# Kernel optimization log

Hardware: AMD Instinct MI355X
Metric: run time of the kernel (lower is better)

The kernel has to match this reference:

```python
import jax, jax.numpy as jnp
import numpy as np

B, T, D_MODEL, D_HEAD = 4, 4096, 512, 64  # batch, token_depth, token_len, d_head
D_K = 64
NEG = -1.0e9  # mask fill value used by the torch module


def setup_inputs() -> dict:
    key = jax.random.key(0)
    kx, kq, kk, kv = jax.random.split(key, 4)
    x = jax.random.normal(kx, (B, T, D_MODEL), dtype=jnp.float32)
    # nn.Linear(token_len, d_head, bias=False) -> weight shape [d_head, token_len]
    Wq = jax.random.normal(kq, (D_HEAD, D_MODEL), dtype=jnp.float32) * 0.02
    Wk = jax.random.normal(kk, (D_HEAD, D_MODEL), dtype=jnp.float32) * 0.02
    Wv = jax.random.normal(kv, (D_HEAD, D_MODEL), dtype=jnp.float32) * 0.02
    return {"x": x, "Wq": Wq, "Wk": Wk, "Wv": Wv}


def reference(x, Wq, Wk, Wv):
    # q/k/v projections: y = x @ W.T  (Linear with bias=False)
    q = jnp.einsum("btd,hd->bth", x, Wq)  # [B,T,D_HEAD]
    k = jnp.einsum("btd,hd->bth", x, Wk)
    v = jnp.einsum("btd,hd->bth", x, Wv)

    scores = jnp.einsum("bth,bsh->bts", q, k)  # [B,T,T]

    # additive causal mask: upper triangle (diagonal=1) filled with -1e9
    t_idx = jnp.arange(T)
    mask = jnp.where(t_idx[None, :] > t_idx[:, None], NEG, 0.0).astype(scores.dtype)
    scores = scores + mask[None, :, :]

    sqrt_dk = jnp.sqrt(jnp.asarray(D_K, dtype=scores.dtype))
    # NOTE: original code applies softmax over dim=1 (the query axis), not -1.
    attn = jax.nn.softmax(scores / sqrt_dk, axis=1)
    out = jnp.einsum("bts,bsh->bth", attn, v)  # [B,T,D_HEAD]
    return out
```

## Files before the change

kernel.cpp:

```cpp
#include <hip/hip_runtime.h>

#define B_ 4
#define T_ 4096
#define DM 512
#define DH 64
#define CS 512
#define CTS 512
#define NTASK 144

typedef short short8 __attribute__((ext_vector_type(8)));
typedef short bf16x4 __attribute__((ext_vector_type(4)));
typedef float f32x4 __attribute__((ext_vector_type(4)));
typedef float float8 __attribute__((ext_vector_type(8)));

__device__ inline short f2bf(float f) {
    unsigned u = __float_as_uint(f);
    u += 0x7fffu + ((u >> 16) & 1u);
    return (short)(u >> 16);
}
__device__ inline float bf2f(short s) {
    return __uint_as_float(((unsigned)(unsigned short)s) << 16);
}
__device__ inline short8 cvt8(const float* p) {
    float8 v = *(const float8*)p;
    short8 r;
#pragma unroll
    for (int j = 0; j < 8; j++) r[j] = f2bf(v[j]);
    return r;
}
__device__ inline unsigned cvt_pk_bf16(float a, float b) {
    unsigned r;
    asm("v_cvt_pk_bf16_f32 %0, %1, %2" : "=v"(r) : "v"(a), "v"(b));
    return r;
}
__device__ inline bf16x4 pmask4(f32x4 d, int sbase, int t) {
    float p[4];
#pragma unroll
    for (int r = 0; r < 4; r++) {
        float e = __expf(d[r] * 0.125f);
        p[r] = (sbase + r <= t) ? e : 0.f;
    }
    union { unsigned u[2]; bf16x4 v; } z;
    z.u[0] = cvt_pk_bf16(p[0], p[1]);
    z.u[1] = cvt_pk_bf16(p[2], p[3]);
    return z.v;
}

__global__ __launch_bounds__(256, 4) void k_proj(
    const float* __restrict__ x, const float* __restrict__ Wq,
    const float* __restrict__ Wk, const float* __restrict__ Wv,
    short* __restrict__ qb, short* __restrict__ kb, short* __restrict__ vb,
    float* __restrict__ lsum)
{
    __shared__ short Xs[16 * 72];
    __shared__ short Ws[192 * 72];
    int tid = threadIdx.x;
    int lane = tid & 63, w = tid >> 6;
    int l16 = lane & 15, quad = lane >> 4;
    int b = blockIdx.x >> 8;
    int tile = blockIdx.x & 255;
    int t0 = tile * 16;
    long xbase = ((long)(b * T_ + t0)) * DM;
    int hb = w * 3;

    if (tid < 16) lsum[blockIdx.x * 16 + tid] = 0.f;

    f32x4 acc[3];
#pragma unroll
    for (int i = 0; i < 3; i++) acc[i] = (f32x4)(0.f);

    for (int kc = 0; kc < DM; kc += 64) {
        if (tid < 128) {
            int row = tid >> 3, col = (tid & 7) * 8;
            *(short8*)(Xs + row * 72 + col) = cvt8(x + xbase + (long)row * DM + kc + col);
        }
#pragma unroll
        for (int p = 0; p < 6; p++) {
            int idx = p * 256 + tid;
            int row = idx >> 3, col = (idx & 7) * 8;
            const float* Wsrc = (p < 2) ? Wq : (p < 4) ? Wk : Wv;
            *(short8*)(Ws + row * 72 + col) = cvt8(Wsrc + (long)(row & 63) * DM + kc + col);
        }
        __syncthreads();
#pragma unroll
        for (int ks = 0; ks < 2; ks++) {
            short8 af = *(const short8*)(Xs + l16 * 72 + ks * 32 + quad * 8);
#pragma unroll
            for (int j = 0; j < 3; j++) {
                short8 bf = *(const short8*)(Ws + ((hb + j) * 16 + l16) * 72 + ks * 32 + quad * 8);
                acc[j] = __builtin_amdgcn_mfma_f32_16x16x32_bf16(af, bf, acc[j], 0, 0, 0);
            }
        }
        __syncthreads();
    }
#pragma unroll
    for (int j = 0; j < 3; j++) {
        int hh = hb + j, m = hh >> 2, h4 = hh & 3;
        short* outp = (m == 0) ? qb : (m == 1) ? kb : vb;
#pragma unroll
        for (int r4 = 0; r4 < 4; r4++) {
            int t = t0 + quad * 4 + r4;
            outp[((long)(b * T_ + t)) * DH + h4 * 16 + l16] = f2bf(acc[j][r4]);
        }
    }
}

__global__ __launch_bounds__(256, 4) void k_stats(
    const short* __restrict__ qb, const short* __restrict__ kb,
    float* __restrict__ lsum, float* __restrict__ out)
{
    __shared__ short Qb[128 * 72];
    int tid = threadIdx.x;
    int lane = tid & 63, w = tid >> 6;
    int l16 = lane & 15, quad = lane >> 4;

    {
        long idx = (long)blockIdx.x * 256 + tid;
        if (idx < 262144) *(f32x4*)(out + idx * 4) = (f32x4)(0.f);
        idx += (long)B_ * NTASK * 256;
        if (idx < 262144) *(f32x4*)(out + idx * 4) = (f32x4)(0.f);
    }

    int b = blockIdx.x / NTASK;
    int m = blockIdx.x - b * NTASK;
    int st = 0, chunk = 0;
    for (st = 0; st < 32; st++) {
        int cnt = 8 - (st >> 2);
        if (m < cnt) { chunk = (st >> 2) + m; break; }
        m -= cnt;
    }
    int c0 = chunk * CTS, cend = c0 + CTS;
    int s0blk = st * 128;
    int s0w = s0blk + w * 32;
    long bq = (long)b * T_ * DH;

    const short8* kp0 = (const short8*)(kb + bq + (long)(s0w + l16) * DH + quad * 8);
    short8 a00 = kp0[0], a01 = kp0[4];
    const short8* kp1 = (const short8*)(kb + bq + (long)(s0w + 16 + l16) * DH + quad * 8);
    short8 a10 = kp1[0], a11 = kp1[4];

    int t_lo = (c0 > s0blk) ? c0 : s0blk;
    int nsteps = (cend - t_lo) >> 7;
    float acc0[4] = {0.f, 0.f, 0.f, 0.f};
    float acc1[4] = {0.f, 0.f, 0.f, 0.f};

    for (int stp = 0; stp < nsteps; stp++) {
        int t0 = t_lo + stp * 128;
#pragma unroll
        for (int p = 0; p < 4; p++) {
            int idx = p * 256 + tid;
            int row = idx >> 3, col = idx & 7;
            *(short8*)(Qb + row * 72 + col * 8) =
                *(const short8*)(qb + bq + (long)(t0 + row) * DH + col * 8);
        }
        __syncthreads();
        for (int sub = 0; sub < 8; sub++) {
            int tt = t0 + sub * 16;
            if (tt + 15 >= s0w) {
                short8 b0 = *(const short8*)(Qb + (sub * 16 + l16) * 72 + quad * 8);
                short8 b1 = *(const short8*)(Qb + (sub * 16 + l16) * 72 + 32 + quad * 8);
                int t = tt + l16;
                f32x4 d0 = (f32x4)(0.f);
                d0 = __builtin_amdgcn_mfma_f32_16x16x32_bf16(a00, b0, d0, 0, 0, 0);
                d0 = __builtin_amdgcn_mfma_f32_16x16x32_bf16(a01, b1, d0, 0, 0, 0);
#pragma unroll
                for (int r = 0; r < 4; r++) {
                    int s = s0w + quad * 4 + r;
                    float p = __expf(d0[r] * 0.125f);
                    acc0[r] += (t >= s) ? p : 0.f;
                }
                if (tt + 15 >= s0w + 16) {
                    f32x4 d1 = (f32x4)(0.f);
                    d1 = __builtin_amdgcn_mfma_f32_16x16x32_bf16(a10, b0, d1, 0, 0, 0);
                    d1 = __builtin_amdgcn_mfma_f32_16x16x32_bf16(a11, b1, d1, 0, 0, 0);
#pragma unroll
                    for (int r = 0; r < 4; r++) {
                        int s = s0w + 16 + quad * 4 + r;
                        float p = __expf(d1[r] * 0.125f);
                        acc1[r] += (t >= s) ? p : 0.f;
                    }
                }
            }
        }
        __syncthreads();
    }
#pragma unroll
    for (int r = 0; r < 4; r++) {
        float v = acc0[r];
        v += __shfl_xor(v, 1, 16); v += __shfl_xor(v, 2, 16);
        v += __shfl_xor(v, 4, 16); v += __shfl_xor(v, 8, 16);
        if (l16 == 0) atomicAdd(&lsum[b * T_ + s0w + quad * 4 + r], v);
        float v1 = acc1[r];
        v1 += __shfl_xor(v1, 1, 16); v1 += __shfl_xor(v1, 2, 16);
        v1 += __shfl_xor(v1, 4, 16); v1 += __shfl_xor(v1, 8, 16);
        if (l16 == 0) atomicAdd(&lsum[b * T_ + s0w + 16 + quad * 4 + r], v1);
    }
}

__global__ __launch_bounds__(256) void k_vt(
    const short* __restrict__ vb, const float* __restrict__ lsum, short* __restrict__ vTc)
{
    int tid = threadIdx.x;
    int b = blockIdx.x >> 6;
    int s0 = (blockIdx.x & 63) * 64;
    int h = tid & 63, g = tid >> 6;
    long vbase = ((long)(b * T_) + s0 + g * 16) * DH + h;
    long lbase = (long)b * T_ + s0 + g * 16;
    short8 lo, hi;
#pragma unroll
    for (int k2 = 0; k2 < 8; k2++) {
        float rl = 1.0f / lsum[lbase + k2];
        lo[k2] = f2bf(bf2f(vb[vbase + (long)k2 * DH]) * rl);
        float rh = 1.0f / lsum[lbase + 8 + k2];
        hi[k2] = f2bf(bf2f(vb[vbase + (long)(8 + k2) * DH]) * rh);
    }
    long ob = ((long)(b * 256 + (s0 >> 4) + g) * 64 + h) * 16;
    *(short8*)(vTc + ob) = lo;
    *(short8*)(vTc + ob + 8) = hi;
}

__global__ __launch_bounds__(256, 4) void k_out(
    const short* __restrict__ qb, const short* __restrict__ kb,
    const short* __restrict__ vTc, float* __restrict__ out)
{
    __shared__ short Kb[128 * 72];
    int tid = threadIdx.x;
    int lane = tid & 63, w = tid >> 6;
    int l16 = lane & 15, quad = lane >> 4;
    int b = blockIdx.x / NTASK;
    int m = blockIdx.x - b * NTASK;
    int strip = 31, chunk = 0;
    for (strip = 31; strip >= 0; strip--) {
        int cnt = (strip >> 2) + 1;
        if (m < cnt) { chunk = m; break; }
        m -= cnt;
    }
    int c0 = chunk * CS;
    int blk_tmax = strip * 128 + 127;
    int s_hi = (c0 + CS < blk_tmax + 1) ? c0 + CS : blk_tmax + 1;
    int nsteps = (s_hi - c0 + 127) >> 7;
    int t0w = strip * 128 + w * 32;
    long bq = (long)b * T_ * DH;

    const short8* qp0 = (const short8*)(qb + bq + (long)(t0w + l16) * DH + quad * 8);
    short8 q00 = qp0[0], q01 = qp0[4];
    const short8* qp1 = (const short8*)(qb + bq + (long)(t0w + 16 + l16) * DH + quad * 8);
    short8 q10 = qp1[0], q11 = qp1[4];
    const short* vTb = vTc + (long)b * (T_ / 16) * DH * 16;

    f32x4 o0[4], o1[4];
#pragma unroll
    for (int i = 0; i < 4; i++) { o0[i] = (f32x4)(0.f); o1[i] = (f32x4)(0.f); }
    int t0 = t0w + l16, t1 = t0 + 16;

    for (int stp = 0; stp < nsteps; stp++) {
        int s0 = c0 + stp * 128;
#pragma unroll
        for (int p = 0; p < 4; p++) {
            int idx = p * 256 + tid;
            int row = idx >> 3, col = idx & 7;
            *(short8*)(Kb + row * 72 + col * 8) =
                *(const short8*)(kb + bq + (long)(s0 + row) * DH + col * 8);
        }
        __syncthreads();

        for (int sub = 0; sub < 8; sub++) {
            int sc = s0 + sub * 16;
            if (sc > t0w + 31) break;
            short8 a0 = *(const short8*)(Kb + (sub * 16 + l16) * 72 + quad * 8);
            short8 a1 = *(const short8*)(Kb + (sub * 16 + l16) * 72 + 32 + quad * 8);
            const short* vc = vTb + (long)(sc >> 4) * 1024 + quad * 4;
            bf16x4 bv[4];
#pragma unroll
            for (int h4 = 0; h4 < 4; h4++)
                bv[h4] = *(const bf16x4*)(vc + (h4 * 16 + l16) * 16);

            f32x4 d1 = (f32x4)(0.f);
            d1 = __builtin_amdgcn_mfma_f32_16x16x32_bf16(a0, q10, d1, 0, 0, 0);
            d1 = __builtin_amdgcn_mfma_f32_16x16x32_bf16(a1, q11, d1, 0, 0, 0);
            bf16x4 pa1 = pmask4(d1, sc + quad * 4, t1);

            bf16x4 pa0 = (bf16x4)(short)0;
            if (sc <= t0w + 15) {
                f32x4 d0 = (f32x4)(0.f);
                d0 = __builtin_amdgcn_mfma_f32_16x16x32_bf16(a0, q00, d0, 0, 0, 0);
                d0 = __builtin_amdgcn_mfma_f32_16x16x32_bf16(a1, q01, d0, 0, 0, 0);
                pa0 = pmask4(d0, sc + quad * 4, t0);
            }
#pragma unroll
            for (int h4 = 0; h4 < 4; h4++) {
                o1[h4] = __builtin_amdgcn_mfma_f32_16x16x16bf16_1k(pa1, bv[h4], o1[h4], 0, 0, 0);
                o0[h4] = __builtin_amdgcn_mfma_f32_16x16x16bf16_1k(pa0, bv[h4], o0[h4], 0, 0, 0);
            }
        }
        __syncthreads();
    }
#pragma unroll
    for (int h4 = 0; h4 < 4; h4++)
#pragma unroll
        for (int r = 0; r < 4; r++) {
            int t = t0w + quad * 4 + r;
            atomicAdd(&out[bq + (long)t * DH + h4 * 16 + l16], o0[h4][r]);
            atomicAdd(&out[bq + (long)(t + 16) * DH + h4 * 16 + l16], o1[h4][r]);
        }
}

extern "C" void kernel_launch(void* const* d_in, const int* in_sizes, int n_in,
                              void* d_out, int out_size, void* d_ws, size_t ws_size,
                              hipStream_t stream) {
    const float* x  = (const float*)d_in[0];
    const float* Wq = (const float*)d_in[1];
    const float* Wk = (const float*)d_in[2];
    const float* Wv = (const float*)d_in[3];
    float* out = (float*)d_out;

    char* ws = (char*)d_ws;
    short* qb   = (short*)(ws);
    short* kb   = (short*)(ws + (2l << 20));
    short* vb   = (short*)(ws + (4l << 20));
    short* vTc  = (short*)(ws + (6l << 20));
    float* lsum = (float*)(ws + (8l << 20));

    k_proj<<<dim3(B_ * T_ / 16), dim3(256), 0, stream>>>(x, Wq, Wk, Wv, qb, kb, vb, lsum);
    k_stats<<<dim3(B_ * NTASK), dim3(256), 0, stream>>>(qb, kb, lsum, out);
    k_vt<<<dim3(B_ * T_ / 64), dim3(256), 0, stream>>>(vb, lsum, vTc);
    k_out<<<dim3(B_ * NTASK), dim3(256), 0, stream>>>(qb, kb, vTc, out);
}
```

Baseline: 143.8 us.

## Use 32-deep bf16 MFMA for PV and double projection tile rows

In k_out, the probability-times-V step moves from the 16x16x16 MFMA to the 16x16x32 MFMA. Keys are processed in chunks of 32, and K rows are permuted as they are loaded into LDS so the score accumulator layout matches the 8-wide A operand. Each lane now loads an 8-element V slice instead of 4. Separately, k_proj handles 32 tokens per block, so each weight tile staged in LDS is reused across twice as many rows, and the grid is halved. The costs are more registers and fewer projection blocks, and the row permutation must match the vT layout exactly to stay correct.

```diff
diff --git a/kernel.cpp b/kernel.cpp
--- a/kernel.cpp
+++ b/kernel.cpp
@@ -45,6 +45,22 @@
     z.u[1] = cvt_pk_bf16(p[2], p[3]);
     return z.v;
 }
+__device__ inline short8 pmask8(f32x4 dlo, f32x4 dhi, int sbase, int t) {
+    float p[8];
+#pragma unroll
+    for (int r = 0; r < 4; r++) {
+        float e = __expf(dlo[r] * 0.125f);
+        p[r] = (sbase + r <= t) ? e : 0.f;
+        float f = __expf(dhi[r] * 0.125f);
+        p[4 + r] = (sbase + 4 + r <= t) ? f : 0.f;
+    }
+    union { unsigned u[4]; short8 v; } z;
+    z.u[0] = cvt_pk_bf16(p[0], p[1]);
+    z.u[1] = cvt_pk_bf16(p[2], p[3]);
+    z.u[2] = cvt_pk_bf16(p[4], p[5]);
+    z.u[3] = cvt_pk_bf16(p[6], p[7]);
+    return z.v;
+}
 
 __global__ __launch_bounds__(256, 4) void k_proj(
     const float* __restrict__ x, const float* __restrict__ Wq,
@@ -52,25 +68,27 @@
     short* __restrict__ qb, short* __restrict__ kb, short* __restrict__ vb,
     float* __restrict__ lsum)
 {
-    __shared__ short Xs[16 * 72];
+    __shared__ short Xs[32 * 72];
     __shared__ short Ws[192 * 72];
     int tid = threadIdx.x;
     int lane = tid & 63, w = tid >> 6;
     int l16 = lane & 15, quad = lane >> 4;
-    int b = blockIdx.x >> 8;
-    int tile = blockIdx.x & 255;
-    int t0 = tile * 16;
+    int b = blockIdx.x >> 7;
+    int tile = blockIdx.x & 127;
+    int t0 = tile * 32;
     long xbase = ((long)(b * T_ + t0)) * DM;
     int hb = w * 3;
 
-    if (tid < 16) lsum[blockIdx.x * 16 + tid] = 0.f;
-
-    f32x4 acc[3];
-#pragma unroll
-    for (int i = 0; i < 3; i++) acc[i] = (f32x4)(0.f);
+    if (tid < 32) lsum[blockIdx.x * 32 + tid] = 0.f;
+
+    f32x4 acc[3][2];
+#pragma unroll
+    for (int i = 0; i < 3; i++)
+#pragma unroll
+        for (int mt = 0; mt < 2; mt++) acc[i][mt] = (f32x4)(0.f);
 
     for (int kc = 0; kc < DM; kc += 64) {
-        if (tid < 128) {
+        {
             int row = tid >> 3, col = (tid & 7) * 8;
             *(short8*)(Xs + row * 72 + col) = cvt8(x + xbase + (long)row * DM + kc + col);
         }
@@ -83,14 +101,16 @@
         }
         __syncthreads();
 #pragma unroll
-        for (int ks = 0; ks < 2; ks++) {
-            short8 af = *(const short8*)(Xs + l16 * 72 + ks * 32 + quad * 8);
-#pragma unroll
-            for (int j = 0; j < 3; j++) {
-                short8 bf = *(const short8*)(Ws + ((hb + j) * 16 + l16) * 72 + ks * 32 + quad * 8);
-                acc[j] = __builtin_amdgcn_mfma_f32_16x16x32_bf16(af, bf, acc[j], 0, 0, 0);
-            }
-        }
+        for (int ks = 0; ks < 2; ks++)
+#pragma unroll
+            for (int mt = 0; mt < 2; mt++) {
+                short8 af = *(const short8*)(Xs + (mt * 16 + l16) * 72 + ks * 32 + quad * 8);
+#pragma unroll
+                for (int j = 0; j < 3; j++) {
+                    short8 bf = *(const short8*)(Ws + ((hb + j) * 16 + l16) * 72 + ks * 32 + quad * 8);
+                    acc[j][mt] = __builtin_amdgcn_mfma_f32_16x16x32_bf16(af, bf, acc[j][mt], 0, 0, 0);
+                }
+            }
         __syncthreads();
     }
 #pragma unroll
@@ -98,10 +118,12 @@
         int hh = hb + j, m = hh >> 2, h4 = hh & 3;
         short* outp = (m == 0) ? qb : (m == 1) ? kb : vb;
 #pragma unroll
-        for (int r4 = 0; r4 < 4; r4++) {
-            int t = t0 + quad * 4 + r4;
-            outp[((long)(b * T_ + t)) * DH + h4 * 16 + l16] = f2bf(acc[j][r4]);
-        }
+        for (int mt = 0; mt < 2; mt++)
+#pragma unroll
+            for (int r4 = 0; r4 < 4; r4++) {
+                int t = t0 + mt * 16 + quad * 4 + r4;
+                outp[((long)(b * T_ + t)) * DH + h4 * 16 + l16] = f2bf(acc[j][mt][r4]);
+            }
     }
 }
 
@@ -259,38 +281,47 @@
         for (int p = 0; p < 4; p++) {
             int idx = p * 256 + tid;
             int row = idx >> 3, col = idx & 7;
+            int mm = row & 31, q2 = mm >> 2, r2 = mm & 3;
+            int pr = (mm < 16) ? (q2 * 8 + r2) : ((q2 - 4) * 8 + r2 + 4);
+            int grow = (row & ~31) | pr;
             *(short8*)(Kb + row * 72 + col * 8) =
-                *(const short8*)(kb + bq + (long)(s0 + row) * DH + col * 8);
-        }
-        __syncthreads();
-
-        for (int sub = 0; sub < 8; sub++) {
-            int sc = s0 + sub * 16;
+                *(const short8*)(kb + bq + (long)(s0 + grow) * DH + col * 8);
+        }
+        __syncthreads();
+
+        for (int sub = 0; sub < 4; sub++) {
+            int sc = s0 + sub * 32;
             if (sc > t0w + 31) break;
-            short8 a0 = *(const short8*)(Kb + (sub * 16 + l16) * 72 + quad * 8);
-            short8 a1 = *(const short8*)(Kb + (sub * 16 + l16) * 72 + 32 + quad * 8);
-            const short* vc = vTb + (long)(sc >> 4) * 1024 + quad * 4;
-            bf16x4 bv[4];
+            short8 a00 = *(const short8*)(Kb + (sub * 32 + l16) * 72 + quad * 8);
+            short8 a01 = *(const short8*)(Kb + (sub * 32 + l16) * 72 + 32 + quad * 8);
+            short8 a10 = *(const short8*)(Kb + (sub * 32 + 16 + l16) * 72 + quad * 8);
+            short8 a11 = *(const short8*)(Kb + (sub * 32 + 16 + l16) * 72 + 32 + quad * 8);
+            const short* vc = vTb + ((long)(sc >> 4) + (quad >> 1)) * 1024 + (quad & 1) * 8;
+            short8 bv[4];
 #pragma unroll
             for (int h4 = 0; h4 < 4; h4++)
-                bv[h4] = *(const bf16x4*)(vc + (h4 * 16 + l16) * 16);
-
-            f32x4 d1 = (f32x4)(0.f);
-            d1 = __builtin_amdgcn_mfma_f32_16x16x32_bf16(a0, q10, d1, 0, 0, 0);
-            d1 = __builtin_amdgcn_mfma_f32_16x16x32_bf16(a1, q11, d1, 0, 0, 0);
-            bf16x4 pa1 = pmask4(d1, sc + quad * 4, t1);
-
-            bf16x4 pa0 = (bf16x4)(short)0;
+                bv[h4] = *(const short8*)(vc + (h4 * 16 + l16) * 16);
+
+            f32x4 dlo = (f32x4)(0.f), dhi = (f32x4)(0.f);
+            dlo = __builtin_amdgcn_mfma_f32_16x16x32_bf16(a00, q10, dlo, 0, 0, 0);
+            dlo = __builtin_amdgcn_mfma_f32_16x16x32_bf16(a01, q11, dlo, 0, 0, 0);
+            dhi = __builtin_amdgcn_mfma_f32_16x16x32_bf16(a10, q10, dhi, 0, 0, 0);
+            dhi = __builtin_amdgcn_mfma_f32_16x16x32_bf16(a11, q11, dhi, 0, 0, 0);
+            short8 pa1 = pmask8(dlo, dhi, sc + 8 * quad, t1);
+
+            short8 pa0 = (short8)(short)0;
             if (sc <= t0w + 15) {
-                f32x4 d0 = (f32x4)(0.f);
-                d0 = __builtin_amdgcn_mfma_f32_16x16x32_bf16(a0, q00, d0, 0, 0, 0);
-                d0 = __builtin_amdgcn_mfma_f32_16x16x32_bf16(a1, q01, d0, 0, 0, 0);
-                pa0 = pmask4(d0, sc + quad * 4, t0);
+                f32x4 elo = (f32x4)(0.f), ehi = (f32x4)(0.f);
+                elo = __builtin_amdgcn_mfma_f32_16x16x32_bf16(a00, q00, elo, 0, 0, 0);
+                elo = __builtin_amdgcn_mfma_f32_16x16x32_bf16(a01, q01, elo, 0, 0, 0);
+                ehi = __builtin_amdgcn_mfma_f32_16x16x32_bf16(a10, q00, ehi, 0, 0, 0);
+                ehi = __builtin_amdgcn_mfma_f32_16x16x32_bf16(a11, q01, ehi, 0, 0, 0);
+                pa0 = pmask8(elo, ehi, sc + 8 * quad, t0);
             }
 #pragma unroll
             for (int h4 = 0; h4 < 4; h4++) {
-                o1[h4] = __builtin_amdgcn_mfma_f32_16x16x16bf16_1k(pa1, bv[h4], o1[h4], 0, 0, 0);
-                o0[h4] = __builtin_amdgcn_mfma_f32_16x16x16bf16_1k(pa0, bv[h4], o0[h4], 0, 0, 0);
+                o1[h4] = __builtin_amdgcn_mfma_f32_16x16x32_bf16(pa1, bv[h4], o1[h4], 0, 0, 0);
+                o0[h4] = __builtin_amdgcn_mfma_f32_16x16x32_bf16(pa0, bv[h4], o0[h4], 0, 0, 0);
             }
         }
         __syncthreads();
@@ -321,7 +352,7 @@
     short* vTc  = (short*)(ws + (6l << 20));
     float* lsum = (float*)(ws + (8l << 20));
 
-    k_proj<<<dim3(B_ * T_ / 16), dim3(256), 0, stream>>>(x, Wq, Wk, Wv, qb, kb, vb, lsum);
+    k_proj<<<dim3(B_ * T_ / 32), dim3(256), 0, stream>>>(x, Wq, Wk, Wv, qb, kb, vb, lsum);
     k_stats<<<dim3(B_ * NTASK), dim3(256), 0, stream>>>(qb, kb, lsum, out);
     k_vt<<<dim3(B_ * T_ / 64), dim3(256), 0, stream>>>(vb, lsum, vTc);
     k_out<<<dim3(B_ * NTASK), dim3(256), 0, stream>>>(qb, kb, vTc, out);
```

Measured after the change: 148.5 us. +3.2%, slower.
